# Optimization experiments

Measured on AMD Instinct MI355X. Metric: run time of the kernel, lower is better.

## Reference

```python
import jax, jax.numpy as jnp
import numpy as np

N = 20000
E = 640000
R = 8          # num_rels == num_bases (basis regularizer with num_bases=-1)
B = 8
IN_SIZE = 128
HID = 256      # 4 * fea_dimen
FEA = 64
TIME = 2880
POI = 12


def setup_inputs() -> dict:
    key = jax.random.key(0)
    ks = jax.random.split(key, 20)
    s = 0.02
    inp = {
        'src': jax.random.randint(ks[0], (E,), 0, N),
        'dst': jax.random.randint(ks[1], (E,), 0, N),
        'etype': jax.random.randint(ks[2], (E,), 0, R),
        'poi_distribution': jax.random.normal(ks[3], (N, POI), jnp.float32),
        'time_distribution': jax.random.normal(ks[4], (N, TIME), jnp.float32),
        'road_feature': jax.random.normal(ks[5], (N, IN_SIZE), jnp.float32),
        # input projections
        'poi_w': jax.random.normal(ks[6], (POI, FEA), jnp.float32) * s,
        'poi_b': jnp.zeros((FEA,), jnp.float32),
        'time_w': jax.random.normal(ks[7], (TIME, 2 * FEA), jnp.float32) * s,
        'time_b': jnp.zeros((2 * FEA,), jnp.float32),
        'road_w': jax.random.normal(ks[8], (IN_SIZE, FEA), jnp.float32) * s,
        'road_b': jnp.zeros((FEA,), jnp.float32),
        # RelGraphConv layer 1 (basis decomposition)
        'basis1': jax.random.normal(ks[9], (B, HID, HID), jnp.float32) * s,
        'coef1': jax.random.normal(ks[10], (R, B), jnp.float32) * s,
        'loop_w1': jax.random.normal(ks[11], (HID, HID), jnp.float32) * s,
        'bias1': jnp.zeros((HID,), jnp.float32),
        # RelGraphConv layer 2
        'basis2': jax.random.normal(ks[12], (B, HID, HID), jnp.float32) * s,
        'coef2': jax.random.normal(ks[13], (R, B), jnp.float32) * s,
        'loop_w2': jax.random.normal(ks[14], (HID, HID), jnp.float32) * s,
        'bias2': jnp.zeros((HID,), jnp.float32),
    }
    return inp


def _rel_graph_conv(h, src, dst, etype, basis, coef, loop_w, bias):
    # W_r = sum_b coef[r,b] * basis[b]  -> (R, HID, HID), small
    W = jnp.einsum('rb,bio->rio', coef, basis)
    # transform every node by every relation weight, then gather per edge
    y = jnp.einsum('ni,rio->nro', h, W)          # (N, R, HID)
    msgs = y[src, etype]                          # (E, HID) gather
    agg = jax.ops.segment_sum(msgs, dst, num_segments=h.shape[0])  # scatter-sum
    return agg + h @ loop_w + bias


def reference(src, dst, etype, poi_distribution, time_distribution, road_feature,
              poi_w, poi_b, time_w, time_b, road_w, road_b,
              basis1, coef1, loop_w1, bias1, basis2, coef2, loop_w2, bias2):
    poi_feat = poi_distribution @ poi_w + poi_b       # (N, 64)
    time_feat = time_distribution @ time_w + time_b   # (N, 128)
    road_feat = road_feature @ road_w + road_b        # (N, 64)
    feat = jnp.concatenate([poi_feat, time_feat, road_feat], axis=1)  # (N, 256)
    h = _rel_graph_conv(feat, src, dst, etype, basis1, coef1, loop_w1, bias1)
    h = jax.nn.relu(h)  # dropout=0.0 -> identity
    h = _rel_graph_conv(h, src, dst, etype, basis2, coef2, loop_w2, bias2)
    return h
```

## Files before the change

kernel.cpp:

```cpp
#include <hip/hip_runtime.h>

#define NN 20000
#define NE 640000
#define NR 8
#define NB 8
#define HID 256
#define KPOI 12
#define KTIME 2880
#define KROAD 128
#define NK (NN * NR)
#define NS 9
#define KCAT (NS * HID)

typedef __attribute__((ext_vector_type(8))) short bf8_t;
typedef __attribute__((ext_vector_type(4))) float f4_t;

__device__ inline unsigned short f2bf(float f) {
  unsigned int u = __float_as_uint(f);
  u += 0x7FFF + ((u >> 16) & 1);
  return (unsigned short)(u >> 16);
}
__device__ inline float bf2f(unsigned short h) {
  return __uint_as_float((unsigned int)h << 16);
}

#define BK 16
__device__ inline void sgemm_body(
    int M, int Nn, int K,
    const float* __restrict__ A, int lda,
    const float* __restrict__ B, int ldb,
    const float* __restrict__ bias,
    unsigned short* __restrict__ C, int ldc, int brow, char* lds)
{
  constexpr int BM = 64, BN = 64, TM = 4, TN = 4;
  constexpr int SA = BM + 4;
  constexpr int SB = BN + 4;
  float* As = (float*)lds;
  float* Bs = (float*)(lds + 4352);
  const int tid = threadIdx.x;
  constexpr int TCOLS = BN / TN;
  const int row0 = (tid / TCOLS) * TM;
  const int col0 = (tid % TCOLS) * TN;

  float acc[TM][TN] = {};

  for (int kb = 0; kb < K; kb += BK) {
    {
      int i = tid;
      int r = i >> 2, q = (i & 3) * 4;
      int grow = brow + r, gk = kb + q;
      if (grow < M && gk + 3 < K) {
        float4 v = *(const float4*)(A + (size_t)grow * lda + gk);
        As[(q + 0) * SA + r] = v.x;
        As[(q + 1) * SA + r] = v.y;
        As[(q + 2) * SA + r] = v.z;
        As[(q + 3) * SA + r] = v.w;
      } else {
#pragma unroll
        for (int j = 0; j < 4; ++j)
          As[(q + j) * SA + r] =
              (grow < M && gk + j < K) ? A[(size_t)grow * lda + gk + j] : 0.f;
      }
    }
    {
      int i = tid;
      int k = i / (BN / 4), cq = (i % (BN / 4)) * 4;
      int gk = kb + k;
      float4 v = {0.f, 0.f, 0.f, 0.f};
      if (gk < K) {
        if (cq + 3 < Nn) {
          v = *(const float4*)(B + (size_t)gk * ldb + cq);
        } else {
#pragma unroll
          for (int j = 0; j < 4; ++j)
            if (cq + j < Nn) (&v.x)[j] = B[(size_t)gk * ldb + cq + j];
        }
      }
      *(float4*)(&Bs[k * SB + cq]) = v;
    }
    __syncthreads();
#pragma unroll
    for (int kk = 0; kk < BK; ++kk) {
      float a[TM], bb[TN];
      *(float4*)(&a[0]) = *(const float4*)(&As[kk * SA + row0]);
      *(float4*)(&bb[0]) = *(const float4*)(&Bs[kk * SB + col0]);
#pragma unroll
      for (int i = 0; i < TM; ++i)
#pragma unroll
        for (int j = 0; j < TN; ++j)
          acc[i][j] += a[i] * bb[j];
    }
    __syncthreads();
  }

  float bcache[TN];
#pragma unroll
  for (int j = 0; j < TN; ++j) bcache[j] = bias[col0 + j];
#pragma unroll
  for (int i = 0; i < TM; ++i) {
    int row = brow + row0 + i;
    if (row >= M) continue;
#pragma unroll
    for (int j = 0; j < TN; ++j)
      C[(size_t)row * ldc + col0 + j] = f2bf(acc[i][j] + bcache[j]);
  }
}

__global__ __launch_bounds__(256) void prep_proj_k(
    const float* __restrict__ loop_w1, const float* __restrict__ loop_w2,
    const float* __restrict__ time_w,
    const float* __restrict__ coef1, const float* __restrict__ basis1,
    const float* __restrict__ coef2, const float* __restrict__ basis2,
    const float* __restrict__ poi_dist, const float* __restrict__ poi_w,
    const float* __restrict__ poi_b,
    const float* __restrict__ road_feat, const float* __restrict__ road_w,
    const float* __restrict__ road_b,
    unsigned short* __restrict__ Wc1, unsigned short* __restrict__ Wc2,
    unsigned short* __restrict__ TWT, unsigned short* __restrict__ hbuf)
{
  __shared__ __align__(16) char lds[8704];
  const int b = blockIdx.x;
  const int to = threadIdx.x & 63;
  const int tq = threadIdx.x >> 6;

  if (b < 378) {
    unsigned short (*T)[66] = (unsigned short (*)[66])lds;
    if (b < 256) {
      const int lr = b >> 4;
      const int tile = b & 15;
      const int i0 = ((tile >> 2) & 3) * 64, o0 = (tile & 3) * 64;
      const float* coef  = (lr < NR) ? coef1 : coef2;
      const float* basis = (lr < NR) ? basis1 : basis2;
      unsigned short* Wc = (lr < NR) ? Wc1 : Wc2;
      const int r = lr & 7;
      float cf[NB];
#pragma unroll
      for (int q = 0; q < NB; ++q) cf[q] = coef[r * NB + q];
#pragma unroll
      for (int k = 0; k < 16; ++k) {
        int i_loc = tq * 16 + k;
        int i = i0 + i_loc;
        float acc = 0.f;
#pragma unroll
        for (int q = 0; q < NB; ++q)
          acc += cf[q] * basis[((size_t)(q * HID + i)) * HID + o0 + to];
        T[i_loc][to] = f2bf(acc);
      }
      __syncthreads();
#pragma unroll
      for (int k = 0; k < 16; ++k) {
        int o_loc = tq * 16 + k;
        Wc[(size_t)(o0 + o_loc) * KCAT + r * HID + i0 + to] = T[to][o_loc];
      }
    } else if (b < 288) {
      const int j = b - 256;
      const int layer = j >> 4;
      const int tile = j & 15;
      const int i0 = ((tile >> 2) & 3) * 64, o0 = (tile & 3) * 64;
      const float* lw = layer ? loop_w2 : loop_w1;
      unsigned short* Wc = layer ? Wc2 : Wc1;
#pragma unroll
      for (int k = 0; k < 16; ++k) {
        int i_loc = tq * 16 + k;
        T[i_loc][to] = f2bf(lw[(size_t)(i0 + i_loc) * HID + o0 + to]);
      }
      __syncthreads();
#pragma unroll
      for (int k = 0; k < 16; ++k) {
        int o_loc = tq * 16 + k;
        Wc[(size_t)(o0 + o_loc) * KCAT + NR * HID + i0 + to] = T[to][o_loc];
      }
    } else {
      const int j = b - 288;
      const int r0 = (j >> 1) * 64, c0 = (j & 1) * 64;
#pragma unroll
      for (int k = 0; k < 16; ++k) {
        int r_loc = tq * 16 + k;
        T[r_loc][to] = f2bf(time_w[(size_t)(r0 + r_loc) * 128 + c0 + to]);
      }
      __syncthreads();
#pragma unroll
      for (int k = 0; k < 16; ++k) {
        int c_loc = tq * 16 + k;
        TWT[(size_t)(c0 + c_loc) * KTIME + r0 + to] = T[to][c_loc];
      }
    }
  } else if (b < 691) {
    sgemm_body(NN, 64, KPOI, poi_dist, KPOI, poi_w, 64, poi_b,
               hbuf + 0, HID, (b - 378) * 64, lds);
  } else {
    sgemm_body(NN, 64, KROAD, road_feat, KROAD, road_w, 64, road_b,
               hbuf + 192, HID, (b - 691) * 64, lds);
  }
}

__global__ __launch_bounds__(512) void mfma_time2(
    const float* __restrict__ A,
    const unsigned short* __restrict__ BT,
    const float* __restrict__ bias,
    unsigned short* __restrict__ featb)
{
  __shared__ __align__(16) char ldsA[2 * 32 * 128];
  __shared__ __align__(16) char ldsB[2 * 128 * 128];
  const int tid = threadIdx.x;
  const int lane = tid & 63;
  const int w = tid >> 6;
  const int g = w >> 2;
  const int cb = w & 3;
  const int brow = blockIdx.x * 32;

  f4_t acc[2][2];
#pragma unroll
  for (int i = 0; i < 2; ++i)
#pragma unroll
    for (int j = 0; j < 2; ++j) acc[i][j] = (f4_t){0.f, 0.f, 0.f, 0.f};

  for (int i = 0; i < 23; ++i) {
    {
      int sg = tid >> 8, r = (tid >> 3) & 31, c8 = tid & 7;
      int step = sg * 23 + i;
      unsigned short hh[8] = {0, 0, 0, 0, 0, 0, 0, 0};
      if (step < 45) {
        const float* ap = A + (size_t)(brow + r) * KTIME + step * 64 + c8 * 8;
        f4_t v0 = *(const f4_t*)ap;
        f4_t v1 = *(const f4_t*)(ap + 4);
#pragma unroll
        for (int j = 0; j < 4; ++j) { hh[j] = f2bf(v0[j]); hh[4 + j] = f2bf(v1[j]); }
      }
      *(bf8_t*)(ldsA + sg * 4096 + r * 128 + ((c8 * 16) ^ ((r & 7) << 4))) =
          *(bf8_t*)hh;
    }
#pragma unroll
    for (int it = 0; it < 4; ++it) {
      int s = tid + it * 512;
      int sg = s >> 10, r = (s >> 3) & 127, c8 = s & 7;
      int step = sg * 23 + i;
      bf8_t v = {0, 0, 0, 0, 0, 0, 0, 0};
      if (step < 45)
        v = *(const bf8_t*)(BT + (size_t)r * KTIME + step * 64 + c8 * 8);
      *(bf8_t*)(ldsB + sg * 16384 + r * 128 + ((c8 * 16) ^ ((r & 7) << 4))) = v;
    }
    __syncthreads();
    if (g * 23 + i < 45) {
#pragma unroll
      for (int ks = 0; ks < 2; ++ks) {
        const int kbyte = ks * 64 + (lane >> 4) * 16;
        bf8_t af[2], bfr[2];
#pragma unroll
        for (int mi = 0; mi < 2; ++mi) {
          int m = mi * 16 + (lane & 15);
          af[mi] = *(const bf8_t*)(
              ldsA + g * 4096 + m * 128 + (kbyte ^ ((m & 7) << 4)));
        }
#pragma unroll
        for (int ni = 0; ni < 2; ++ni) {
          int n = cb * 32 + ni * 16 + (lane & 15);
          bfr[ni] = *(const bf8_t*)(
              ldsB + g * 16384 + n * 128 + (kbyte ^ ((n & 7) << 4)));
        }
#pragma unroll
        for (int mi = 0; mi < 2; ++mi)
#pragma unroll
          for (int ni = 0; ni < 2; ++ni)
            acc[mi][ni] = __builtin_amdgcn_mfma_f32_16x16x32_bf16(
                af[mi], bfr[ni], acc[mi][ni], 0, 0, 0);
      }
    }
    __syncthreads();
  }

  float* rb = (float*)ldsB;
  if (g == 1) {
#pragma unroll
    for (int mi = 0; mi < 2; ++mi)
#pragma unroll
      for (int ni = 0; ni < 2; ++ni)
#pragma unroll
        for (int j = 0; j < 4; ++j)
          rb[(cb * 64 + lane) * 16 + (mi * 2 + ni) * 4 + j] = acc[mi][ni][j];
  }
  __syncthreads();
  if (g == 0) {
    const int rq = (lane >> 4) * 4;
    const int cl = lane & 15;
#pragma unroll
    for (int ni = 0; ni < 2; ++ni) {
      int c = cb * 32 + ni * 16 + cl;
      float bv = bias[c];
#pragma unroll
      for (int mi = 0; mi < 2; ++mi) {
#pragma unroll
        for (int j = 0; j < 4; ++j) {
          float v = acc[mi][ni][j] +
                    rb[(cb * 64 + lane) * 16 + (mi * 2 + ni) * 4 + j] + bv;
          int row = brow + mi * 16 + rq + j;
          featb[(size_t)row * 256 + 64 + c] = f2bf(v);
        }
      }
    }
  }
}

__global__ __launch_bounds__(256) void agg_k(
    const int* __restrict__ offs, const unsigned short* __restrict__ ssrc,
    const unsigned short* __restrict__ hin, unsigned short* __restrict__ Zc) {
  int d = (blockIdx.x * 256 + threadIdx.x) >> 6;
  int lane = threadIdx.x & 63;
  if (d >= NN) return;
  unsigned short* zrow = Zc + (size_t)d * KCAT;
  *(ushort4*)(zrow + NR * HID + lane * 4) =
      *(const ushort4*)(hin + (size_t)d * HID + lane * 4);
  int ob[NR + 1];
#pragma unroll
  for (int r = 0; r <= NR; ++r) ob[r] = offs[d * NR + r];
#pragma unroll 1
  for (int q = 0; q < NR; ++q) {
    int e = ob[q], hi = ob[q + 1];
    f4_t az = {0.f, 0.f, 0.f, 0.f};
    for (; e + 4 <= hi; e += 4) {
      int s0 = ssrc[e], s1 = ssrc[e + 1], s2 = ssrc[e + 2], s3 = ssrc[e + 3];
      ushort4 u0 = *(const ushort4*)(hin + (size_t)s0 * HID + lane * 4);
      ushort4 u1 = *(const ushort4*)(hin + (size_t)s1 * HID + lane * 4);
      ushort4 u2 = *(const ushort4*)(hin + (size_t)s2 * HID + lane * 4);
      ushort4 u3 = *(const ushort4*)(hin + (size_t)s3 * HID + lane * 4);
      az.x += (bf2f(u0.x) + bf2f(u1.x)) + (bf2f(u2.x) + bf2f(u3.x));
      az.y += (bf2f(u0.y) + bf2f(u1.y)) + (bf2f(u2.y) + bf2f(u3.y));
      az.z += (bf2f(u0.z) + bf2f(u1.z)) + (bf2f(u2.z) + bf2f(u3.z));
      az.w += (bf2f(u0.w) + bf2f(u1.w)) + (bf2f(u2.w) + bf2f(u3.w));
    }
    for (; e < hi; ++e) {
      int s = ssrc[e];
      ushort4 u = *(const ushort4*)(hin + (size_t)s * HID + lane * 4);
      az.x += bf2f(u.x); az.y += bf2f(u.y);
      az.z += bf2f(u.z); az.w += bf2f(u.w);
    }
    unsigned short hz[4] = {f2bf(az.x), f2bf(az.y), f2bf(az.z), f2bf(az.w)};
    *(ushort4*)(zrow + q * HID + lane * 4) = *(ushort4*)hz;
  }
}

template<int EPI>
__global__ __launch_bounds__(512) void gemm_cat(
    const unsigned short* __restrict__ Zc,
    const unsigned short* __restrict__ Wc,
    const float* __restrict__ bias,
    float* __restrict__ C, unsigned short* __restrict__ hb)
{
  __shared__ __align__(16) char At[64 * 128];
  __shared__ __align__(16) char Bt[256 * 128];
  const int tid = threadIdx.x;
  const int lane = tid & 63;
  const int w = tid >> 6;
  const int wm = w >> 2;
  const int wn = w & 3;
  const int brow = blockIdx.x * 64;

  f4_t acc[2][4];
#pragma unroll
  for (int i = 0; i < 2; ++i)
#pragma unroll
    for (int j = 0; j < 4; ++j) acc[i][j] = (f4_t){0.f, 0.f, 0.f, 0.f};

  for (int kb = 0; kb < KCAT; kb += 64) {
    {
      int r = tid >> 3, c8 = tid & 7;
      int grow = brow + r;
      bf8_t v = {0, 0, 0, 0, 0, 0, 0, 0};
      if (grow < NN) v = *(const bf8_t*)(Zc + (size_t)grow * KCAT + kb + c8 * 8);
      *(bf8_t*)(At + r * 128 + ((c8 * 16) ^ ((r & 7) << 4))) = v;
    }
#pragma unroll
    for (int it = 0; it < 4; ++it) {
      int slot = tid + it * 512;
      int n = slot >> 3, c8 = slot & 7;
      bf8_t v = *(const bf8_t*)(Wc + (size_t)n * KCAT + kb + c8 * 8);
      *(bf8_t*)(Bt + n * 128 + ((c8 * 16) ^ ((n & 7) << 4))) = v;
    }
    __syncthreads();
#pragma unroll
    for (int ks = 0; ks < 2; ++ks) {
      const int kbyte = ks * 64 + (lane >> 4) * 16;
      bf8_t af[2], bfr[4];
#pragma unroll
      for (int mi = 0; mi < 2; ++mi) {
        int m = wm * 32 + mi * 16 + (lane & 15);
        af[mi] = *(const bf8_t*)(At + m * 128 + (kbyte ^ ((m & 7) << 4)));
      }
#pragma unroll
      for (int ni = 0; ni < 4; ++ni) {
        int n = wn * 64 + ni * 16 + (lane & 15);
        bfr[ni] = *(const bf8_t*)(Bt + n * 128 + (kbyte ^ ((n & 7) << 4)));
      }
#pragma unroll
      for (int mi = 0; mi < 2; ++mi)
#pragma unroll
        for (int ni = 0; ni < 4; ++ni)
          acc[mi][ni] = __builtin_amdgcn_mfma_f32_16x16x32_bf16(
              af[mi], bfr[ni], acc[mi][ni], 0, 0, 0);
    }
    __syncthreads();
  }

  const int rq = (lane >> 4) * 4;
  const int cl = lane & 15;
#pragma unroll
  for (int ni = 0; ni < 4; ++ni) {
    int c = wn * 64 + ni * 16 + cl;
    float bv = bias[c];
#pragma unroll
    for (int mi = 0; mi < 2; ++mi) {
#pragma unroll
      for (int j = 0; j < 4; ++j) {
        int row = brow + wm * 32 + mi * 16 + rq + j;
        if (row < NN) {
          size_t o = (size_t)row * HID + c;
          float v = acc[mi][ni][j] + bv;
          if (EPI == 0) C[o] = v;
          else          hb[o] = f2bf(fmaxf(v, 0.f));
        }
      }
    }
  }
}

__global__ __launch_bounds__(256) void hist_k(const int* __restrict__ dst,
                                              const int* __restrict__ et,
                                              int* __restrict__ counts) {
  int e = blockIdx.x * 256 + threadIdx.x;
  if (e < NE) atomicAdd(&counts[dst[e] * NR + et[e]], 1);
}

__global__ __launch_bounds__(256) void scan_all(
    const int* __restrict__ counts, int* __restrict__ offs,
    int* __restrict__ cursor, int* __restrict__ bsums,
    int* __restrict__ counter) {
  __shared__ int sh[256];
  __shared__ int base_sh;
  const int bid = blockIdx.x;
  const int t = threadIdx.x;
  const int gbase = bid * 1024;
  int v[4], run[4];
  int s = 0;
#pragma unroll
  for (int j = 0; j < 4; ++j) {
    int idx = gbase + t * 4 + j;
    v[j] = (idx < NK) ? counts[idx] : 0;
    s += v[j];
  }
  sh[t] = s;
  __syncthreads();
  for (int off = 1; off < 256; off <<= 1) {
    int x = (t >= off) ? sh[t - off] : 0;
    __syncthreads();
    sh[t] += x;
    __syncthreads();
  }
  {
    int r = sh[t] - s;
#pragma unroll
    for (int j = 0; j < 4; ++j) { run[j] = r; r += v[j]; }
  }
  if (t == 255) {
    bsums[bid] = sh[255];
    __threadfence();
    atomicAdd(counter, 1);
  }
  if (t == 0) {
    while (atomicAdd(counter, 0) < (int)gridDim.x) {}
    __threadfence();
    int b = 0;
    for (int j = 0; j < bid; ++j) b += atomicAdd(&bsums[j], 0);
    base_sh = b;
  }
  __syncthreads();
  const int base = base_sh;
#pragma unroll
  for (int j = 0; j < 4; ++j) {
    int idx = gbase + t * 4 + j;
    if (idx < NK) {
      int val = run[j] + base;
      offs[idx] = val;
      cursor[idx] = val;
    }
  }
  if (bid == 0 && t == 0) offs[NK] = NE;
}

__global__ __launch_bounds__(256) void fill_k(const int* __restrict__ src,
                                              const int* __restrict__ dst,
                                              const int* __restrict__ et,
                                              int* __restrict__ cursor,
                                              unsigned short* __restrict__ ssrc) {
  int e = blockIdx.x * 256 + threadIdx.x;
  if (e < NE) {
    int key = dst[e] * NR + et[e];
    int p = atomicAdd(&cursor[key], 1);
    ssrc[p] = (unsigned short)src[e];
  }
}

extern "C" void kernel_launch(void* const* d_in, const int* in_sizes, int n_in,
                              void* d_out, int out_size, void* d_ws, size_t ws_size,
                              hipStream_t stream) {
  const int*   srcp      = (const int*)d_in[0];
  const int*   dstp      = (const int*)d_in[1];
  const int*   etypep    = (const int*)d_in[2];
  const float* poi_dist  = (const float*)d_in[3];
  const float* time_dist = (const float*)d_in[4];
  const float* road_feat = (const float*)d_in[5];
  const float* poi_w     = (const float*)d_in[6];
  const float* poi_b     = (const float*)d_in[7];
  const float* time_w    = (const float*)d_in[8];
  const float* time_b    = (const float*)d_in[9];
  const float* road_w    = (const float*)d_in[10];
  const float* road_b    = (const float*)d_in[11];
  const float* basis1    = (const float*)d_in[12];
  const float* coef1     = (const float*)d_in[13];
  const float* loop_w1   = (const float*)d_in[14];
  const float* bias1     = (const float*)d_in[15];
  const float* basis2    = (const float*)d_in[16];
  const float* coef2     = (const float*)d_in[17];
  const float* loop_w2   = (const float*)d_in[18];
  const float* bias2     = (const float*)d_in[19];

  float* out = (float*)d_out;

  char* ws = (char*)d_ws;
  unsigned short* Wc1    = (unsigned short*)(ws);
  unsigned short* Wc2    = (unsigned short*)(ws + 1179648);
  unsigned short* TWT    = (unsigned short*)(ws + 2359296);
  unsigned short* hbuf   = (unsigned short*)(ws + 3096576);
  unsigned short* Zcat   = (unsigned short*)(ws + 13336576);
  int*            offs   = (int*)  (ws + 105496576);
  int*            bsums  = (int*)  (ws + 106136592);
  unsigned short* ssrc   = (unsigned short*)(ws + 106137616);
  int*            cursor = (int*)  (ws + 107417616);
  int*            counts = (int*)Zcat;
  int*            counter = counts + NK;

  dim3 blk(256);

  hipMemsetAsync(counts, 0, (NK + 1) * sizeof(int), stream);
  hist_k<<<NE / 256, blk, 0, stream>>>(dstp, etypep, counts);
  scan_all<<<(NK + 1023) / 1024, blk, 0, stream>>>(counts, offs, cursor,
                                                   bsums, counter);
  fill_k<<<NE / 256, blk, 0, stream>>>(srcp, dstp, etypep, cursor, ssrc);

  prep_proj_k<<<1004, blk, 0, stream>>>(loop_w1, loop_w2, time_w,
                                        coef1, basis1, coef2, basis2,
                                        poi_dist, poi_w, poi_b,
                                        road_feat, road_w, road_b,
                                        Wc1, Wc2, TWT, hbuf);

  mfma_time2<<<NN / 32, 512, 0, stream>>>(time_dist, TWT, time_b, hbuf);

  agg_k<<<NN * 64 / 256, blk, 0, stream>>>(offs, ssrc, hbuf, Zcat);
  gemm_cat<1><<<(NN + 63) / 64, 512, 0, stream>>>(Zcat, Wc1, bias1, nullptr, hbuf);

  agg_k<<<NN * 64 / 256, blk, 0, stream>>>(offs, ssrc, hbuf, Zcat);
  gemm_cat<0><<<(NN + 63) / 64, 512, 0, stream>>>(Zcat, Wc2, bias2, out, nullptr);
}
```

Before: 399.5 us.

## Fuse CSR build into one persistent kernel and use direct global-to-LDS loads

Replaces the memset plus histogram, scan and fill kernels with a single persistent kernel of 157 blocks that uses software grid barriers between phases, removing several launches. It also switches the B-tile loads in the time GEMM, and the A and B tile loads in the concat GEMM, to global_load_lds 16-byte transfers with a lane-swizzled source column to keep the XOR LDS layout. This bypasses register staging. The grid barriers rely on all blocks being co-resident, and with so few blocks the histogram and fill phases may have less parallelism than the 2500-block kernels they replace.

```diff
diff --git a/kernel.cpp b/kernel.cpp
--- a/kernel.cpp
+++ b/kernel.cpp
@@ -22,6 +22,88 @@
 }
 __device__ inline float bf2f(unsigned short h) {
   return __uint_as_float((unsigned int)h << 16);
+}
+
+__device__ inline void gl_lds16(const void* g, void* l) {
+  __builtin_amdgcn_global_load_lds(
+      (const __attribute__((address_space(1))) void*)g,
+      (__attribute__((address_space(3))) void*)l, 16, 0, 0);
+}
+
+__device__ inline void gbar(int* c, int nb) {
+  __syncthreads();
+  if (threadIdx.x == 0) {
+    __threadfence();
+    atomicAdd(c, 1);
+    while (atomicAdd(c, 0) < nb) {}
+    __threadfence();
+  }
+  __syncthreads();
+}
+
+__global__ __launch_bounds__(256) void csr_build(
+    const int* __restrict__ src, const int* __restrict__ dst,
+    const int* __restrict__ et,
+    int* __restrict__ counts, int* __restrict__ offs,
+    int* __restrict__ cursor, int* __restrict__ bsums,
+    int* __restrict__ ctr, unsigned short* __restrict__ ssrc)
+{
+  __shared__ int sh[256];
+  __shared__ int base_sh;
+  const int bid = blockIdx.x, t = threadIdx.x;
+  const int nb = gridDim.x;
+  const int gt = bid * 256 + t, gn = nb * 256;
+
+  for (int i = gt; i < NK; i += gn) counts[i] = 0;
+  gbar(ctr + 0, nb);
+  for (int e = gt; e < NE; e += gn)
+    atomicAdd(&counts[dst[e] * NR + et[e]], 1);
+  gbar(ctr + 1, nb);
+  int v[4], run[4];
+  {
+    int s = 0;
+#pragma unroll
+    for (int j = 0; j < 4; ++j) {
+      int idx = bid * 1024 + t * 4 + j;
+      v[j] = (idx < NK) ? atomicAdd(&counts[idx], 0) : 0;
+      s += v[j];
+    }
+    sh[t] = s;
+    __syncthreads();
+    for (int off = 1; off < 256; off <<= 1) {
+      int x = (t >= off) ? sh[t - off] : 0;
+      __syncthreads();
+      sh[t] += x;
+      __syncthreads();
+    }
+    int r = sh[t] - s;
+#pragma unroll
+    for (int j = 0; j < 4; ++j) { run[j] = r; r += v[j]; }
+    if (t == 255) bsums[bid] = sh[255];
+  }
+  gbar(ctr + 2, nb);
+  if (t == 0) {
+    int b = 0;
+    for (int j = 0; j < bid; ++j) b += atomicAdd(&bsums[j], 0);
+    base_sh = b;
+  }
+  __syncthreads();
+#pragma unroll
+  for (int j = 0; j < 4; ++j) {
+    int idx = bid * 1024 + t * 4 + j;
+    if (idx < NK) {
+      int val = run[j] + base_sh;
+      offs[idx] = val;
+      cursor[idx] = val;
+    }
+  }
+  if (bid == 0 && t == 0) offs[NK] = NE;
+  gbar(ctr + 3, nb);
+  for (int e = gt; e < NE; e += gn) {
+    int key = dst[e] * NR + et[e];
+    int p = atomicAdd(&cursor[key], 1);
+    ssrc[p] = (unsigned short)src[e];
+  }
 }
 
 #define BK 16
@@ -208,6 +290,7 @@
   const int g = w >> 2;
   const int cb = w & 3;
   const int brow = blockIdx.x * 32;
+  const int c8sw = (lane & 7) ^ (lane >> 3);
 
   f4_t acc[2][2];
 #pragma unroll
@@ -232,13 +315,15 @@
     }
 #pragma unroll
     for (int it = 0; it < 4; ++it) {
-      int s = tid + it * 512;
-      int sg = s >> 10, r = (s >> 3) & 127, c8 = s & 7;
+      int s0 = (w << 6) + it * 512;
+      int sg = s0 >> 10;
+      int r0 = (s0 >> 3) & 127;
       int step = sg * 23 + i;
-      bf8_t v = {0, 0, 0, 0, 0, 0, 0, 0};
-      if (step < 45)
-        v = *(const bf8_t*)(BT + (size_t)r * KTIME + step * 64 + c8 * 8);
-      *(bf8_t*)(ldsB + sg * 16384 + r * 128 + ((c8 * 16) ^ ((r & 7) << 4))) = v;
+      if (step < 45) {
+        int r = r0 + (lane >> 3);
+        gl_lds16(BT + (size_t)r * KTIME + step * 64 + c8sw * 8,
+                 ldsB + sg * 16384 + r0 * 128);
+      }
     }
     __syncthreads();
     if (g * 23 + i < 45) {
@@ -354,6 +439,8 @@
   const int wm = w >> 2;
   const int wn = w & 3;
   const int brow = blockIdx.x * 64;
+  const bool full = (brow + 64 <= NN);
+  const int c8sw = (lane & 7) ^ (lane >> 3);
 
   f4_t acc[2][4];
 #pragma unroll
@@ -362,7 +449,11 @@
     for (int j = 0; j < 4; ++j) acc[i][j] = (f4_t){0.f, 0.f, 0.f, 0.f};
 
   for (int kb = 0; kb < KCAT; kb += 64) {
-    {
+    if (full) {
+      int row = (w << 3) + (lane >> 3);
+      gl_lds16(Zc + (size_t)(brow + row) * KCAT + kb + c8sw * 8,
+               At + (w << 10));
+    } else {
       int r = tid >> 3, c8 = tid & 7;
       int grow = brow + r;
       bf8_t v = {0, 0, 0, 0, 0, 0, 0, 0};
@@ -371,10 +462,9 @@
     }
 #pragma unroll
     for (int it = 0; it < 4; ++it) {
-      int slot = tid + it * 512;
-      int n = slot >> 3, c8 = slot & 7;
-      bf8_t v = *(const bf8_t*)(Wc + (size_t)n * KCAT + kb + c8 * 8);
-      *(bf8_t*)(Bt + n * 128 + ((c8 * 16) ^ ((n & 7) << 4))) = v;
+      int n0 = (w << 3) + it * 64;
+      int n = n0 + (lane >> 3);
+      gl_lds16(Wc + (size_t)n * KCAT + kb + c8sw * 8, Bt + n0 * 128);
     }
     __syncthreads();
 #pragma unroll
@@ -420,82 +510,6 @@
         }
       }
     }
-  }
-}
-
-__global__ __launch_bounds__(256) void hist_k(const int* __restrict__ dst,
-                                              const int* __restrict__ et,
-                                              int* __restrict__ counts) {
-  int e = blockIdx.x * 256 + threadIdx.x;
-  if (e < NE) atomicAdd(&counts[dst[e] * NR + et[e]], 1);
-}
-
-__global__ __launch_bounds__(256) void scan_all(
-    const int* __restrict__ counts, int* __restrict__ offs,
-    int* __restrict__ cursor, int* __restrict__ bsums,
-    int* __restrict__ counter) {
-  __shared__ int sh[256];
-  __shared__ int base_sh;
-  const int bid = blockIdx.x;
-  const int t = threadIdx.x;
-  const int gbase = bid * 1024;
-  int v[4], run[4];
-  int s = 0;
-#pragma unroll
-  for (int j = 0; j < 4; ++j) {
-    int idx = gbase + t * 4 + j;
-    v[j] = (idx < NK) ? counts[idx] : 0;
-    s += v[j];
-  }
-  sh[t] = s;
-  __syncthreads();
-  for (int off = 1; off < 256; off <<= 1) {
-    int x = (t >= off) ? sh[t - off] : 0;
-    __syncthreads();
-    sh[t] += x;
-    __syncthreads();
-  }
-  {
-    int r = sh[t] - s;
-#pragma unroll
-    for (int j = 0; j < 4; ++j) { run[j] = r; r += v[j]; }
-  }
-  if (t == 255) {
-    bsums[bid] = sh[255];
-    __threadfence();
-    atomicAdd(counter, 1);
-  }
-  if (t == 0) {
-    while (atomicAdd(counter, 0) < (int)gridDim.x) {}
-    __threadfence();
-    int b = 0;
-    for (int j = 0; j < bid; ++j) b += atomicAdd(&bsums[j], 0);
-    base_sh = b;
-  }
-  __syncthreads();
-  const int base = base_sh;
-#pragma unroll
-  for (int j = 0; j < 4; ++j) {
-    int idx = gbase + t * 4 + j;
-    if (idx < NK) {
-      int val = run[j] + base;
-      offs[idx] = val;
-      cursor[idx] = val;
-    }
-  }
-  if (bid == 0 && t == 0) offs[NK] = NE;
-}
-
-__global__ __launch_bounds__(256) void fill_k(const int* __restrict__ src,
-                                              const int* __restrict__ dst,
-                                              const int* __restrict__ et,
-                                              int* __restrict__ cursor,
-                                              unsigned short* __restrict__ ssrc) {
-  int e = blockIdx.x * 256 + threadIdx.x;
-  if (e < NE) {
-    int key = dst[e] * NR + et[e];
-    int p = atomicAdd(&cursor[key], 1);
-    ssrc[p] = (unsigned short)src[e];
   }
 }
 
@@ -535,16 +549,14 @@
   int*            bsums  = (int*)  (ws + 106136592);
   unsigned short* ssrc   = (unsigned short*)(ws + 106137616);
   int*            cursor = (int*)  (ws + 107417616);
+  int*            ctr    = (int*)  (ws + 108057616);
   int*            counts = (int*)Zcat;
-  int*            counter = counts + NK;
 
   dim3 blk(256);
 
-  hipMemsetAsync(counts, 0, (NK + 1) * sizeof(int), stream);
-  hist_k<<<NE / 256, blk, 0, stream>>>(dstp, etypep, counts);
-  scan_all<<<(NK + 1023) / 1024, blk, 0, stream>>>(counts, offs, cursor,
-                                                   bsums, counter);
-  fill_k<<<NE / 256, blk, 0, stream>>>(srcp, dstp, etypep, cursor, ssrc);
+  hipMemsetAsync(ctr, 0, 16, stream);
+  csr_build<<<(NK + 1023) / 1024, blk, 0, stream>>>(
+      srcp, dstp, etypep, counts, offs, cursor, bsums, ctr, ssrc);
 
   prep_proj_k<<<1004, blk, 0, stream>>>(loop_w1, loop_w2, time_w,
                                         coef1, basis1, coef2, basis2,
```

New measurement: 422.2 us. 5.7% more time.
